# Kernel optimization log

Hardware: AMD Instinct MI355X
Metric: run time of the kernel (lower is better)

Reference implementation:

```python
import jax, jax.numpy as jnp
import numpy as np

B, S, E, H, DH, F, L, C = 32, 197, 768, 12, 64, 2048, 4, 1000
LN_EPS = 1e-5


def setup_inputs() -> dict:
    key = jax.random.key(0)
    ks = jax.random.split(key, 16)
    sc = 0.02
    return {
        "x": jax.random.normal(ks[0], (B, S, E), dtype=jnp.float32),
        "Wk": jax.random.normal(ks[1], (L, H, E, DH), dtype=jnp.float32) * sc,
        "Wq": jax.random.normal(ks[2], (L, H, E, DH), dtype=jnp.float32) * sc,
        "Wv": jax.random.normal(ks[3], (L, H, E, DH), dtype=jnp.float32) * sc,
        "Wconv": jax.random.normal(ks[4], (L, H * DH, E), dtype=jnp.float32) * sc,
        "ln1_w": jnp.ones((L, E), jnp.float32),
        "ln1_b": jnp.zeros((L, E), jnp.float32),
        "ln2_w": jnp.ones((L, E), jnp.float32),
        "ln2_b": jnp.zeros((L, E), jnp.float32),
        "W1": jax.random.normal(ks[5], (L, E, F), dtype=jnp.float32) * sc,
        "b1": jnp.zeros((L, F), jnp.float32),
        "W2": jax.random.normal(ks[6], (L, F, E), dtype=jnp.float32) * sc,
        "b2": jnp.zeros((L, E), jnp.float32),
        "Wc": jax.random.normal(ks[7], (E, C), dtype=jnp.float32) * sc,
        "bc": jnp.zeros((C,), jnp.float32),
    }


def _layernorm(x, w, b):
    mu = jnp.mean(x, axis=-1, keepdims=True)
    var = jnp.mean(jnp.square(x - mu), axis=-1, keepdims=True)
    return (x - mu) * jax.lax.rsqrt(var + LN_EPS) * w + b


def reference(x, Wk, Wq, Wv, Wconv, ln1_w, ln1_b, ln2_w, ln2_b, W1, b1, W2, b2, Wc, bc):
    # NOTE: original scales attention scores by sqrt(seq_len), not sqrt(d_k)
    seq_len = x.shape[1]
    inv_scale = 1.0 / jnp.sqrt(jnp.float32(seq_len))
    h = x
    for l in range(L):  # small fixed layer loop
        xn = _layernorm(h, ln1_w[l], ln1_b[l])
        q = jnp.einsum('bse,hed->bhsd', xn, Wq[l])
        k = jnp.einsum('bse,hed->bhsd', xn, Wk[l])
        v = jnp.einsum('bse,hed->bhsd', xn, Wv[l])
        scores = jnp.einsum('bhsd,bhtd->bhst', q, k) * inv_scale
        att = jax.nn.softmax(scores, axis=-1)
        o = jnp.einsum('bhst,bhtd->bhsd', att, v)
        # concat heads: b s (h d), head index outermost in last dim
        o = o.transpose(0, 2, 1, 3).reshape(o.shape[0], o.shape[2], H * DH)
        mha = o @ Wconv[l]
        res1 = mha + h
        xn2 = _layernorm(res1, ln2_w[l], ln2_b[l])
        ff = jax.nn.gelu(xn2 @ W1[l] + b1[l], approximate=False) @ W2[l] + b2[l]
        h = ff + res1
    logits = h[:, 0] @ Wc + bc
    return jax.nn.softmax(logits, axis=-1)
```

## Files before the change

### kernel.cpp

```cpp
#include <hip/hip_runtime.h>
#include <hip/hip_bf16.h>
#include <math.h>

#define BQ 32
#define SQ 197
#define EQ 768
#define HQ 12
#define DHQ 64
#define FQ 2048
#define LQ 4
#define CQ 1000
#define BSQ (BQ*SQ)
#define SP 208
#define S16 13
#define MP (BQ*SP)
#define QKV3 2304
#define KTP 7
#define LN_EPS 1e-5f

typedef __bf16 bf16x8 __attribute__((ext_vector_type(8)));
typedef float f32x4 __attribute__((ext_vector_type(4)));
typedef unsigned short u16x8 __attribute__((ext_vector_type(8)));

typedef const __attribute__((address_space(1))) unsigned int* gas_t;
typedef __attribute__((address_space(3))) unsigned int* las_t;

__device__ __forceinline__ __hip_bfloat16 tobf(float f) { return __float2bfloat16(f); }

__device__ __forceinline__ size_t pk(int rt, int KT, int kt, int lane) {
    return (((size_t)rt * KT + kt) * 64 + (size_t)lane) * 8;
}

#define QPK_SLAB (S16*2*512)
#define QPK_TOT  ((size_t)BQ*HQ*QPK_SLAB + 4096)
#define VPK_SLAB (4*KTP*512)
#define VPK_TOT  ((size_t)BQ*HQ*VPK_SLAB + 4096)
#define LWSLAB (4*(size_t)EQ*EQ + 2*(size_t)EQ*FQ)

template<int N>
__device__ __forceinline__ void waitvm() {
    asm volatile("s_waitcnt vmcnt(%0)" :: "n"(N) : "memory");
}
__device__ __forceinline__ void barx() {
    asm volatile("" ::: "memory");
    __builtin_amdgcn_s_barrier();
    asm volatile("" ::: "memory");
}
__device__ __forceinline__ void lds_fence() {
    asm volatile("s_waitcnt lgkmcnt(0)" ::: "memory");
    __builtin_amdgcn_sched_barrier(0);
}

__device__ __forceinline__ float gelu_f(float v) {
    float ax = fabsf(v) * 0.70710678118654752f;
    float t  = __builtin_amdgcn_rcpf(1.0f + 0.3275911f * ax);
    float p  = ((((1.061405429f * t - 1.453152027f) * t + 1.421413741f) * t
               - 0.284496736f) * t + 0.254829592f) * t;
    float e  = __expf(-ax * ax);
    float er = 1.0f - p * e;
    return v * (0.5f * (1.0f + copysignf(er, v)));
}

__global__ __launch_bounds__(256) void copy_pad(const float* __restrict__ x,
    float* __restrict__ bh)
{
    int r = blockIdx.x;
    int b = r / SP, s = r - b * SP;
    float* dst = bh + (size_t)r * EQ;
    int t = threadIdx.x;
    if (s < SQ) {
        const float* src = x + ((size_t)b * SQ + s) * EQ;
        dst[t]       = src[t];
        dst[t + 256] = src[t + 256];
        dst[t + 512] = src[t + 512];
    } else {
        dst[t] = 0.f; dst[t + 256] = 0.f; dst[t + 512] = 0.f;
    }
}

__device__ __forceinline__ void tconv_body(const float* __restrict__ ip,
    unsigned short* __restrict__ out, int C, int KT, int ntb_base, int r0, int c0)
{
    __shared__ float tile[64][65];
    int t = threadIdx.x;
    int tc = t & 63, tr = t >> 6;
    #pragma unroll
    for (int p = 0; p < 16; ++p) {
        int r = p * 4 + tr;
        tile[r][tc] = ip[(size_t)(r0 + r) * C + c0 + tc];
    }
    __syncthreads();
    int ntb = ntb_base + (c0 >> 4);
    int ktb = r0 >> 5;
    #pragma unroll
    for (int p = 0; p < 2; ++p) {
        int cc = p * 256 + t;
        int lane = cc & 63, grp = cc >> 6;
        int ktl = grp & 1, ntl = grp >> 1;
        int er = ktl * 32 + (lane >> 4) * 8;
        int dc = ntl * 16 + (lane & 15);
        u16x8 v;
        #pragma unroll
        for (int e = 0; e < 8; ++e) {
            __hip_bfloat16 h = tobf(tile[er + e][dc]);
            v[e] = *(unsigned short*)&h;
        }
        *(u16x8*)(out + pk(ntb + ntl, KT, ktb + ktl, lane)) = v;
    }
}

__global__ __launch_bounds__(256) void tconv_all(
    const float* __restrict__ Wq, const float* __restrict__ Wk,
    const float* __restrict__ Wv, const float* __restrict__ Wcv,
    const float* __restrict__ W1, const float* __restrict__ W2,
    unsigned short* __restrict__ wAll)
{
    int id = blockIdx.x;
    const int l = id / 1344; id -= l * 1344;
    unsigned short* wl = wAll + (size_t)l * LWSLAB;
    const float* src; unsigned short* dst;
    int C, KT, ntb, r0, c0;
    if (id < 432) {
        int x = id % 12, z = id / 12;
        int which = z / 12, zz = z - which * 12;
        const float* s0 = (which == 0) ? Wq : (which == 1) ? Wk : Wv;
        src = s0 + ((size_t)l * HQ + zz) * EQ * DHQ;
        dst = wl + (size_t)which * EQ * EQ;
        C = DHQ; KT = 24; ntb = zz * 4; r0 = x * 64; c0 = 0;
    } else if (id < 576) {
        int t = id - 432;
        src = Wcv + (size_t)l * EQ * EQ;
        dst = wl + 3 * (size_t)EQ * EQ;
        C = EQ; KT = 24; ntb = 0; r0 = (t % 12) * 64; c0 = (t / 12) * 64;
    } else if (id < 960) {
        int t = id - 576;
        src = W1 + (size_t)l * EQ * FQ;
        dst = wl + 4 * (size_t)EQ * EQ;
        C = FQ; KT = 24; ntb = 0; r0 = (t % 12) * 64; c0 = (t / 12) * 64;
    } else {
        int t = id - 960;
        src = W2 + (size_t)l * FQ * EQ;
        dst = wl + 4 * (size_t)EQ * EQ + (size_t)EQ * FQ;
        C = EQ; KT = 64; ntb = 0; r0 = (t % 32) * 64; c0 = (t / 32) * 64;
    }
    tconv_body(src, dst, C, KT, ntb, r0, c0);
}

__global__ __launch_bounds__(256) void ln_kernel(const float* __restrict__ in,
    const float* __restrict__ w, const float* __restrict__ b,
    unsigned short* __restrict__ out)
{
    const int wv = threadIdx.x >> 6, L = threadIdx.x & 63;
    const int row = blockIdx.x * 4 + wv;
    const float* x = in + (size_t)row * EQ;
    float4 a0 = *(const float4*)(x + 8 * L);
    float4 a1 = *(const float4*)(x + 8 * L + 4);
    float4 a2 = make_float4(0.f, 0.f, 0.f, 0.f), a3 = a2;
    const bool two = (L < 32);
    if (two) {
        a2 = *(const float4*)(x + 512 + 8 * L);
        a3 = *(const float4*)(x + 512 + 8 * L + 4);
    }
    float s = a0.x + a0.y + a0.z + a0.w + a1.x + a1.y + a1.z + a1.w
            + a2.x + a2.y + a2.z + a2.w + a3.x + a3.y + a3.z + a3.w;
    #pragma unroll
    for (int d = 1; d < 64; d <<= 1) s += __shfl_xor(s, d);
    const float mu = s * (1.0f / EQ);
    float q = (a0.x-mu)*(a0.x-mu) + (a0.y-mu)*(a0.y-mu) + (a0.z-mu)*(a0.z-mu) + (a0.w-mu)*(a0.w-mu)
            + (a1.x-mu)*(a1.x-mu) + (a1.y-mu)*(a1.y-mu) + (a1.z-mu)*(a1.z-mu) + (a1.w-mu)*(a1.w-mu);
    if (two)
        q += (a2.x-mu)*(a2.x-mu) + (a2.y-mu)*(a2.y-mu) + (a2.z-mu)*(a2.z-mu) + (a2.w-mu)*(a2.w-mu)
           + (a3.x-mu)*(a3.x-mu) + (a3.y-mu)*(a3.y-mu) + (a3.z-mu)*(a3.z-mu) + (a3.w-mu)*(a3.w-mu);
    #pragma unroll
    for (int d = 1; d < 64; d <<= 1) q += __shfl_xor(q, d);
    const float rs = rsqrtf(q * (1.0f / EQ) + LN_EPS);

    const int rt = row >> 4, rsl = row & 15;
    auto store_chunk = [&](int c, float4 v0, float4 v1) {
        int kt = c >> 2, c2 = c & 3;
        int lane2 = (c2 << 4) + rsl;
        int k0 = c << 3;
        float4 w0 = *(const float4*)(w + k0), w1 = *(const float4*)(w + k0 + 4);
        float4 g0 = *(const float4*)(b + k0), g1 = *(const float4*)(b + k0 + 4);
        float va[8] = {v0.x, v0.y, v0.z, v0.w, v1.x, v1.y, v1.z, v1.w};
        float wa[8] = {w0.x, w0.y, w0.z, w0.w, w1.x, w1.y, w1.z, w1.w};
        float ba[8] = {g0.x, g0.y, g0.z, g0.w, g1.x, g1.y, g1.z, g1.w};
        u16x8 o;
        #pragma unroll
        for (int e = 0; e < 8; ++e) {
            __hip_bfloat16 h = tobf((va[e] - mu) * rs * wa[e] + ba[e]);
            o[e] = *(unsigned short*)&h;
        }
        *(u16x8*)(out + pk(rt, 24, kt, lane2)) = o;
    };
    store_chunk(L, a0, a1);
    if (two) store_chunk(64 + L, a2, a3);
}

template<int KT, int RT>
__device__ __forceinline__ void kloop_staged(
    const unsigned short* __restrict__ Apk,
    const unsigned short* __restrict__ Bpk,
    int rtb, int ntb, int tid, unsigned short* sm, f32x4 (&acc)[RT][4])
{
    static_assert(KT >= 3, "need >=3 k-tiles");
    constexpr int AC  = RT * 2;
    constexpr int NCH = AC + 8;
    constexpr int CPW = NCH / 4;
    const int lane = tid & 63, w = tid >> 6;
    const int wr = w >> 1, wc = w & 1;
    const int cbase = w * CPW;

    const unsigned short* sp[CPW];
    #pragma unroll
    for (int q = 0; q < CPW; ++q) {
        int c = cbase + q;
        sp[q] = (c < AC) ? Apk + pk(rtb + c, KT, 0, lane)
                         : Bpk + pk(ntb + (c - AC), KT, 0, lane);
    }
    unsigned short* bufs0 = sm;
    unsigned short* bufs1 = sm + NCH * 512;
    unsigned short* bufs2 = sm + 2 * NCH * 512;

    auto stagef = [&](unsigned short* dst) {
        #pragma unroll
        for (int q = 0; q < CPW; ++q) {
            __builtin_amdgcn_global_load_lds(
                (gas_t)sp[q], (las_t)(dst + (cbase + q) * 512), 16, 0, 0);
            sp[q] += 512;
        }
    };
    auto frags = [&](const unsigned short* cur, bf16x8 (&af)[RT], bf16x8 (&bb)[4]) {
        #pragma unroll
        for (int i = 0; i < RT; ++i)
            af[i] = *(const bf16x8*)(cur + (wr * RT + i) * 512 + lane * 8);
        #pragma unroll
        for (int j = 0; j < 4; ++j)
            bb[j] = *(const bf16x8*)(cur + (AC + wc * 4 + j) * 512 + lane * 8);
    };
    auto mf = [&](bf16x8 (&af)[RT], bf16x8 (&bb)[4]) {
        #pragma unroll
        for (int i = 0; i < RT; ++i)
            #pragma unroll
            for (int j = 0; j < 4; ++j)
                acc[i][j] = __builtin_amdgcn_mfma_f32_16x16x32_bf16(af[i], bb[j], acc[i][j], 0, 0, 0);
    };

    stagef(bufs0);
    stagef(bufs1);
    unsigned short *cur = bufs0, *nxt = bufs1, *nx2 = bufs2;

    #pragma unroll 1
    for (int kt = 0; kt < KT - 2; ++kt) {
        waitvm<CPW>();
        barx();
        bf16x8 af[RT], bb[4];
        frags(cur, af, bb);
        stagef(nx2);
        mf(af, bb);
        unsigned short* t_ = cur; cur = nxt; nxt = nx2; nx2 = t_;
    }
    {
        waitvm<CPW>();
        barx();
        bf16x8 af[RT], bb[4];
        frags(cur, af, bb);
        mf(af, bb);
        cur = nxt;
    }
    {
        waitvm<0>();
        barx();
        bf16x8 af[RT], bb[4];
        frags(cur, af, bb);
        mf(af, bb);
    }
}

enum { EPI_NONE = 0, EPI_RES = 1, EPI_BIAS_GELU = 2, EPI_BIAS_RES = 3, EPI_QKV = 4 };

template<int EPI, int KT, int RT>
__global__ __launch_bounds__(256, 3) void mgemm_pk(
    const unsigned short* __restrict__ Apk, const unsigned short* __restrict__ Bpk,
    void* __restrict__ Cm, const float* __restrict__ bias,
    const float* __restrict__ res, int N, int nNT)
{
    constexpr int NCH = RT * 2 + 8;
    __shared__ __align__(16) unsigned short smem[(3 * NCH * 1024) / 2];

    const int nRowT = (RT == 4) ? 52 : 104;
    const int g = blockIdx.x & 7;
    const int sIdx = blockIdx.x >> 3;
    const int b0 = (nRowT * g) >> 3, b1 = (nRowT * (g + 1)) >> 3;
    const int colT = sIdx % nNT, rloc = sIdx / nNT;
    if (b0 + rloc >= b1) return;
    const int row0 = (b0 + rloc) * (RT * 32), col0 = colT << 7;

    const int tid = threadIdx.x;
    const int lane = tid & 63;
    const int w = tid >> 6;
    const int wr = w >> 1, wc = w & 1;
    const int l15 = lane & 15, quad = lane >> 4;

    f32x4 acc[RT][4] = {};
    kloop_staged<KT, RT>(Apk, Bpk, row0 >> 4, col0 >> 4, tid, smem, acc);

    if constexpr (EPI == EPI_BIAS_GELU) {
        __syncthreads();
        auto Cs = (unsigned short (*)[136])smem;
        #pragma unroll
        for (int j = 0; j < 4; ++j) {
            float bv = bias[col0 + wc * 64 + j * 16 + l15];
            #pragma unroll
            for (int i = 0; i < RT; ++i)
                #pragma unroll
                for (int rg = 0; rg < 4; ++rg) {
                    float v = gelu_f(acc[i][j][rg] + bv);
                    __hip_bfloat16 h = tobf(v);
                    Cs[wr * 64 + i * 16 + quad * 4 + rg][wc * 64 + j * 16 + l15] =
                        *(unsigned short*)&h;
                }
        }
        __syncthreads();
        const int KT2 = N >> 5;
        #pragma unroll
        for (int p = 0; p < 8; ++p) {
            int cc = p * 256 + tid;
            int ln2 = cc & 63, grp = cc >> 6;
            int ktl = grp & 3, rtl = grp >> 2;
            int rowl = rtl * 16 + (ln2 & 15);
            u16x8 v;
            #pragma unroll
            for (int e = 0; e < 8; ++e)
                v[e] = Cs[rowl][ktl * 32 + (ln2 >> 4) * 8 + e];
            *(u16x8*)((unsigned short*)Cm + pk((row0 >> 4) + rtl, KT2, (col0 >> 5) + ktl, ln2)) = v;
        }
    } else if constexpr (EPI == EPI_QKV) {
        unsigned short* qpk = (unsigned short*)Cm;
        unsigned short* kpk = (unsigned short*)(void*)bias;
        unsigned short* vpk = (unsigned short*)(void*)res;
        __syncthreads();
        auto Cs = (unsigned short (*)[136])smem;
        #pragma unroll
        for (int j = 0; j < 4; ++j)
            #pragma unroll
            for (int i = 0; i < 4; ++i)
                #pragma unroll
                for (int rg = 0; rg < 4; ++rg) {
                    __hip_bfloat16 h = tobf(acc[i][j][rg]);
                    Cs[wr * 64 + i * 16 + quad * 4 + rg][wc * 64 + j * 16 + l15] =
                        *(unsigned short*)&h;
                }
        __syncthreads();

        const int treg = col0 >> 7;
        if (treg < 12) {
            unsigned short* dst = (treg < 6) ? qpk : kpk;
            const int h0 = ((col0 % 768) >> 6);
            #pragma unroll
            for (int p = 0; p < 8; ++p) {
                int cc = p * 256 + tid;
                int ln2 = cc & 63, grp = cc >> 6;
                int hl = grp & 1, kt = (grp >> 1) & 1, rtl = grp >> 2;
                int row16 = (row0 >> 4) + rtl;
                int bb = row16 / S16;
                int s16 = row16 - bb * S16;
                int h = h0 + hl;
                u16x8 v;
                #pragma unroll
                for (int e = 0; e < 8; ++e)
                    v[e] = Cs[rtl * 16 + (ln2 & 15)][hl * 64 + kt * 32 + (ln2 >> 4) * 8 + e];
                *(u16x8*)(dst + ((((size_t)(bb * HQ + h) * S16 + s16) * 2 + kt) << 9) + ln2 * 8) = v;
            }
        } else {
            const int h0 = (col0 - 1536) >> 6;
            #pragma unroll
            for (int p = 0; p < 8; ++p) {
                int cc = p * 256 + tid;
                int dloc = cc & 127;
                int g8 = cc >> 7;
                int gr = row0 + g8 * 8;
                int bb = gr / SP;
                int tl = gr - bb * SP;
                int tt = tl >> 5;
                int tsub = (tl >> 3) & 3;
                int h = h0 + (dloc >> 6);
                int dt = (dloc >> 4) & 3;
                int lane2 = tsub * 16 + (dloc & 15);
                u16x8 v;
                #pragma unroll
                for (int e = 0; e < 8; ++e)
                    v[e] = Cs[g8 * 8 + e][dloc];
                *(u16x8*)(vpk + (size_t)(bb * HQ + h) * VPK_SLAB + pk(dt, KTP, tt, lane2)) = v;
            }
        }
    } else {
        #pragma unroll
        for (int j = 0; j < 4; ++j) {
            int c = col0 + wc * 64 + j * 16 + l15;
            float bv = (EPI == EPI_BIAS_RES) ? bias[c] : 0.f;
            #pragma unroll
            for (int i = 0; i < RT; ++i)
                #pragma unroll
                for (int rg = 0; rg < 4; ++rg) {
                    int r = row0 + wr * (RT * 16) + i * 16 + quad * 4 + rg;
                    float v = acc[i][j][rg];
                    size_t idx = (size_t)r * N + c;
                    if (EPI == EPI_BIAS_RES) {
                        ((float*)Cm)[idx] = v + bv + res[idx];
                    } else if (EPI == EPI_RES) {
                        ((float*)Cm)[idx] = v + res[idx];
                    } else {
                        ((__hip_bfloat16*)Cm)[idx] = tobf(v);
                    }
                }
        }
    }
}

__global__ __launch_bounds__(128, 4) void attn_fused(
    const unsigned short* __restrict__ qpk, const unsigned short* __restrict__ kpk,
    const unsigned short* __restrict__ vpk, unsigned short* __restrict__ opk)
{
    __shared__ unsigned short Ps[2][16][240];
    __shared__ unsigned short Cs[2][16][72];
    const int bh = blockIdx.x;
    const int b = bh / HQ, h = bh - b * HQ;
    const int tid = threadIdx.x;
    const int w = tid >> 6, lane = tid & 63;
    const int l15 = lane & 15, quad = lane >> 4;
    const int rt = blockIdx.y * 2 + w;
    if (rt >= S16) return;

    const unsigned short* qs = qpk + (size_t)bh * QPK_SLAB;
    const unsigned short* ks = kpk + (size_t)bh * QPK_SLAB;
    const unsigned short* vs = vpk + (size_t)bh * VPK_SLAB;

    bf16x8 af0 = *(const bf16x8*)(qs + ((rt * 2 + 0) << 9) + lane * 8);
    bf16x8 af1 = *(const bf16x8*)(qs + ((rt * 2 + 1) << 9) + lane * 8);

    f32x4 acc[13] = {};
    bf16x8 kc0 = *(const bf16x8*)(ks + (0 << 9) + lane * 8);
    bf16x8 kc1 = *(const bf16x8*)(ks + (1 << 9) + lane * 8);
    #pragma unroll
    for (int j = 0; j < 13; ++j) {
        bf16x8 kn0, kn1;
        if (j + 1 < 13) {
            kn0 = *(const bf16x8*)(ks + (((j + 1) * 2 + 0) << 9) + lane * 8);
            kn1 = *(const bf16x8*)(ks + (((j + 1) * 2 + 1) << 9) + lane * 8);
        }
        __builtin_amdgcn_s_setprio(1);
        acc[j] = __builtin_amdgcn_mfma_f32_16x16x32_bf16(af0, kc0, acc[j], 0, 0, 0);
        acc[j] = __builtin_amdgcn_mfma_f32_16x16x32_bf16(af1, kc1, acc[j], 0, 0, 0);
        __builtin_amdgcn_s_setprio(0);
        kc0 = kn0; kc1 = kn1;
    }

    bf16x8 vb[4];
    #pragma unroll
    for (int d = 0; d < 4; ++d)
        vb[d] = *(const bf16x8*)(vs + pk(d, KTP, 0, lane));

    const float scale = 0.07124704998790965f;
    const int xr = (quad & 2) << 3;
    const unsigned short zbf = 0;
    float inv[4];
    #pragma unroll
    for (int rg = 0; rg < 4; ++rg) {
        float y[13];
        float m = -1e30f;
        #pragma unroll
        for (int j = 0; j < 13; ++j) {
            float v = acc[j][rg] * scale;
            if (j == 12) v = (l15 < 5) ? v : -1e30f;
            y[j] = v;
            m = fmaxf(m, v);
        }
        #pragma unroll
        for (int d = 1; d < 16; d <<= 1) m = fmaxf(m, __shfl_xor(m, d));
        float s = 0.f;
        #pragma unroll
        for (int j = 0; j < 13; ++j) {
            float e = __expf(y[j] - m);
            s += e;
            __hip_bfloat16 hv = tobf(e);
            Ps[w][quad * 4 + rg][(j * 16 + l15) ^ xr] = *(unsigned short*)&hv;
        }
        Ps[w][quad * 4 + rg][(208 + l15) ^ xr] = zbf;
        #pragma unroll
        for (int d = 1; d < 16; d <<= 1) s += __shfl_xor(s, d);
        inv[rg] = 1.0f / s;
    }
    lds_fence();

    f32x4 av[4] = {};
    #pragma unroll
    for (int kk = 0; kk < KTP; ++kk) {
        bf16x8 vn[4];
        if (kk + 1 < KTP) {
            #pragma unroll
            for (int d = 0; d < 4; ++d)
                vn[d] = *(const bf16x8*)(vs + pk(d, KTP, kk + 1, lane));
        }
        int col = (kk * 32 + quad * 8) ^ ((l15 & 8) << 1);
        bf16x8 pf = *(const bf16x8*)&Ps[w][l15][col];
        __builtin_amdgcn_s_setprio(1);
        #pragma unroll
        for (int d = 0; d < 4; ++d)
            av[d] = __builtin_amdgcn_mfma_f32_16x16x32_bf16(pf, vb[d], av[d], 0, 0, 0);
        __builtin_amdgcn_s_setprio(0);
        #pragma unroll
        for (int d = 0; d < 4; ++d) vb[d] = vn[d];
    }

    #pragma unroll
    for (int d = 0; d < 4; ++d)
        #pragma unroll
        for (int rg = 0; rg < 4; ++rg) {
            __hip_bfloat16 hv = tobf(av[d][rg] * inv[rg]);
            Cs[w][quad * 4 + rg][d * 16 + l15] = *(unsigned short*)&hv;
        }
    lds_fence();

    const int rtg = b * S16 + rt;
    #pragma unroll
    for (int ktl = 0; ktl < 2; ++ktl) {
        u16x8 v;
        #pragma unroll
        for (int e = 0; e < 8; ++e)
            v[e] = Cs[w][l15][ktl * 32 + quad * 8 + e];
        *(u16x8*)(opk + pk(rtg, 24, h * 2 + ktl, lane)) = v;
    }
}

__global__ __launch_bounds__(256) void logits_kernel(
    const float* __restrict__ hbuf, const float* __restrict__ Wc,
    const float* __restrict__ bc, float* __restrict__ logits)
{
    __shared__ __align__(16) float hs[768];
    __shared__ float red[256];
    int b = blockIdx.y;
    int tid = threadIdx.x;
    const float* hr = hbuf + (size_t)b * SP * EQ;
    for (int p = tid; p < 192; p += 256)
        *(float4*)&hs[p << 2] = *(const float4*)(hr + (p << 2));
    __syncthreads();
    int cl = tid & 31, ks = tid >> 5;
    int c = blockIdx.x * 32 + cl;
    int cs = (c < CQ) ? c : 0;
    float s = 0.f;
    int e0 = ks * 96;
    #pragma unroll 8
    for (int e = 0; e < 96; ++e)
        s = fmaf(hs[e0 + e], Wc[(size_t)(e0 + e) * CQ + cs], s);
    red[tid] = s;
    __syncthreads();
    for (int off = 128; off >= 32; off >>= 1) {
        if (tid < off) red[tid] += red[tid + off];
        __syncthreads();
    }
    if (tid < 32 && c < CQ)
        logits[(size_t)b * CQ + c] = red[tid] + bc[c];
}

__global__ __launch_bounds__(256) void smax_kernel(
    const float* __restrict__ logits, float* __restrict__ out)
{
    __shared__ float red[256];
    int b = blockIdx.x;
    int t = threadIdx.x;
    const float* lp = logits + (size_t)b * CQ;
    float lg[4];
    #pragma unroll
    for (int j = 0; j < 4; ++j) {
        int c = t + j * 256;
        lg[j] = (c < CQ) ? lp[c] : -1e30f;
    }
    float m = fmaxf(fmaxf(lg[0], lg[1]), fmaxf(lg[2], lg[3]));
    red[t] = m;
    __syncthreads();
    for (int off = 128; off; off >>= 1) {
        if (t < off) red[t] = fmaxf(red[t], red[t + off]);
        __syncthreads();
    }
    m = red[0];
    __syncthreads();
    float ex[4], s = 0.f;
    #pragma unroll
    for (int j = 0; j < 4; ++j) {
        ex[j] = (t + j * 256 < CQ) ? __expf(lg[j] - m) : 0.f;
        s += ex[j];
    }
    red[t] = s;
    __syncthreads();
    for (int off = 128; off; off >>= 1) {
        if (t < off) red[t] += red[t + off];
        __syncthreads();
    }
    float inv = 1.0f / red[0];
    #pragma unroll
    for (int j = 0; j < 4; ++j)
        if (t + j * 256 < CQ) out[(size_t)b * CQ + t + j * 256] = ex[j] * inv;
}

extern "C" void kernel_launch(void* const* d_in, const int* in_sizes, int n_in,
                              void* d_out, int out_size, void* d_ws, size_t ws_size,
                              hipStream_t stream)
{
    const float* x     = (const float*)d_in[0];
    const float* Wk    = (const float*)d_in[1];
    const float* Wq    = (const float*)d_in[2];
    const float* Wv    = (const float*)d_in[3];
    const float* Wconv = (const float*)d_in[4];
    const float* ln1w  = (const float*)d_in[5];
    const float* ln1b  = (const float*)d_in[6];
    const float* ln2w  = (const float*)d_in[7];
    const float* ln2b  = (const float*)d_in[8];
    const float* W1    = (const float*)d_in[9];
    const float* b1    = (const float*)d_in[10];
    const float* W2    = (const float*)d_in[11];
    const float* b2    = (const float*)d_in[12];
    const float* Wc    = (const float*)d_in[13];
    const float* bc    = (const float*)d_in[14];
    float* out = (float*)d_out;

    const size_t MPE = (size_t)MP * EQ;

    float* w = (float*)d_ws;
    float* bh    = w; w += MPE;
    float* res1  = w; w += MPE;
    float* logit = w; w += (size_t)BQ * CQ;
    unsigned short* qpk  = (unsigned short*)w;
    unsigned short* kpk  = qpk + QPK_TOT;
    unsigned short* vpk  = kpk + QPK_TOT;
    unsigned short* actb = vpk + VPK_TOT;
    unsigned short* ffh  = actb + MPE;
    unsigned short* wAll = ffh + (size_t)MP * FQ;

    copy_pad<<<MP, 256, 0, stream>>>(x, bh);
    tconv_all<<<4 * 1344, 256, 0, stream>>>(Wq, Wk, Wv, Wconv, W1, W2, wAll);

    for (int l = 0; l < LQ; ++l) {
        unsigned short* wl   = wAll + (size_t)l * LWSLAB;
        unsigned short* WcvT = wl + 3 * (size_t)EQ * EQ;
        unsigned short* W1T  = wl + 4 * (size_t)EQ * EQ;
        unsigned short* W2T  = W1T + (size_t)EQ * FQ;

        ln_kernel<<<MP / 4, 256, 0, stream>>>(bh, ln1w + l * EQ, ln1b + l * EQ, actb);

        mgemm_pk<EPI_QKV, 24, 4><<<8 * 7 * 18, 256, 0, stream>>>(
            actb, wl, qpk, (const float*)kpk, (const float*)vpk, QKV3, 18);

        attn_fused<<<dim3(BQ * HQ, 7), 128, 0, stream>>>(qpk, kpk, vpk, actb);

        mgemm_pk<EPI_RES, 24, 2><<<8 * 13 * 6, 256, 0, stream>>>(
            actb, WcvT, res1, nullptr, bh, EQ, 6);

        ln_kernel<<<MP / 4, 256, 0, stream>>>(res1, ln2w + l * EQ, ln2b + l * EQ, actb);

        mgemm_pk<EPI_BIAS_GELU, 24, 4><<<8 * 7 * 16, 256, 0, stream>>>(
            actb, W1T, ffh, b1 + l * FQ, nullptr, FQ, 16);
        mgemm_pk<EPI_BIAS_RES, 64, 2><<<8 * 13 * 6, 256, 0, stream>>>(
            ffh, W2T, bh, b2 + l * EQ, res1, EQ, 6);
    }
    logits_kernel<<<dim3(32, BQ), 256, 0, stream>>>(bh, Wc, bc, logit);
    smax_kernel<<<BQ, 256, 0, stream>>>(logit, out);
}
```

Measured before the change: 710.5 us.

## Add 512x128-tile GEMM kernel with triple-buffered LDS staging for QKV and FFN1

Adds a new GEMM kernel using 512-thread blocks that compute a 512x128 output tile. It stages A and B chunks into LDS with direct global-to-LDS loads and a three-deep buffer ring, and the epilogue is written out in four 128-row bands through shared memory. The QKV projection and the first FFN GEMM now use this kernel instead of the 128-row-tile kernel, with the aim of reusing each weight tile across more rows and cutting global reads of B. In exchange there are far fewer blocks (234 and 208), large LDS use and heavy register pressure from 32 accumulators per wave, which can hurt occupancy and load balance.

```diff
diff --git a/kernel.cpp b/kernel.cpp
--- a/kernel.cpp
+++ b/kernel.cpp
@@ -305,116 +305,198 @@
     f32x4 acc[RT][4] = {};
     kloop_staged<KT, RT>(Apk, Bpk, row0 >> 4, col0 >> 4, tid, smem, acc);
 
-    if constexpr (EPI == EPI_BIAS_GELU) {
+    #pragma unroll
+    for (int j = 0; j < 4; ++j) {
+        int c = col0 + wc * 64 + j * 16 + l15;
+        float bv = (EPI == EPI_BIAS_RES) ? bias[c] : 0.f;
+        #pragma unroll
+        for (int i = 0; i < RT; ++i)
+            #pragma unroll
+            for (int rg = 0; rg < 4; ++rg) {
+                int r = row0 + wr * (RT * 16) + i * 16 + quad * 4 + rg;
+                float v = acc[i][j][rg];
+                size_t idx = (size_t)r * N + c;
+                if (EPI == EPI_BIAS_RES) {
+                    ((float*)Cm)[idx] = v + bv + res[idx];
+                } else if (EPI == EPI_RES) {
+                    ((float*)Cm)[idx] = v + res[idx];
+                } else {
+                    ((__hip_bfloat16*)Cm)[idx] = tobf(v);
+                }
+            }
+    }
+}
+
+template<int EPI, int KT>
+__global__ __launch_bounds__(512, 2) void mgemm_big(
+    const unsigned short* __restrict__ Apk, const unsigned short* __restrict__ Bpk,
+    void* __restrict__ Cm, const float* __restrict__ bias,
+    const float* __restrict__ res, int N, int nNT)
+{
+    constexpr int NCH = 40;
+    __shared__ __align__(16) unsigned short smem[3 * NCH * 512];
+
+    const int sIdx = blockIdx.x;
+    const int colT = sIdx % nNT, mt = sIdx / nNT;
+    const int row0 = mt << 9, col0 = colT << 7;
+
+    const int tid = threadIdx.x;
+    const int lane = tid & 63;
+    const int w = tid >> 6;
+    const int wr = w >> 1, wc = w & 1;
+    const int l15 = lane & 15, quad = lane >> 4;
+    const int rtb = row0 >> 4, ntb = col0 >> 4;
+
+    const unsigned short* sp[5];
+    #pragma unroll
+    for (int q = 0; q < 5; ++q) {
+        int c = w * 5 + q;
+        sp[q] = (c < 32) ? Apk + pk(rtb + c, KT, 0, lane)
+                         : Bpk + pk(ntb + (c - 32), KT, 0, lane);
+    }
+    unsigned short* bufs0 = smem;
+    unsigned short* bufs1 = smem + NCH * 512;
+    unsigned short* bufs2 = smem + 2 * NCH * 512;
+
+    auto stagef = [&](unsigned short* dst) {
+        #pragma unroll
+        for (int q = 0; q < 5; ++q) {
+            __builtin_amdgcn_global_load_lds(
+                (gas_t)sp[q], (las_t)(dst + (w * 5 + q) * 512), 16, 0, 0);
+            sp[q] += 512;
+        }
+    };
+    f32x4 acc[8][4] = {};
+    auto ldfrags = [&](const unsigned short* cur, bf16x8 (&af)[8], bf16x8 (&bb)[4]) {
+        #pragma unroll
+        for (int i = 0; i < 8; ++i)
+            af[i] = *(const bf16x8*)(cur + (wr * 8 + i) * 512 + lane * 8);
+        #pragma unroll
+        for (int j = 0; j < 4; ++j)
+            bb[j] = *(const bf16x8*)(cur + (32 + wc * 4 + j) * 512 + lane * 8);
+    };
+    auto domfma = [&](bf16x8 (&af)[8], bf16x8 (&bb)[4]) {
+        __builtin_amdgcn_s_setprio(1);
+        #pragma unroll
+        for (int i = 0; i < 8; ++i)
+            #pragma unroll
+            for (int j = 0; j < 4; ++j)
+                acc[i][j] = __builtin_amdgcn_mfma_f32_16x16x32_bf16(af[i], bb[j], acc[i][j], 0, 0, 0);
+        __builtin_amdgcn_s_setprio(0);
+    };
+
+    stagef(bufs0);
+    stagef(bufs1);
+    unsigned short *cur = bufs0, *nxt = bufs1, *nx2 = bufs2;
+    #pragma unroll 1
+    for (int kt = 0; kt < KT - 2; ++kt) {
+        waitvm<5>();
+        barx();
+        bf16x8 af[8], bb[4];
+        ldfrags(cur, af, bb);
+        stagef(nx2);
+        domfma(af, bb);
+        unsigned short* t_ = cur; cur = nxt; nxt = nx2; nx2 = t_;
+    }
+    {
+        waitvm<5>();
+        barx();
+        bf16x8 af[8], bb[4];
+        ldfrags(cur, af, bb);
+        domfma(af, bb);
+        cur = nxt;
+    }
+    {
+        waitvm<0>();
+        barx();
+        bf16x8 af[8], bb[4];
+        ldfrags(cur, af, bb);
+        domfma(af, bb);
+    }
+
+    __syncthreads();
+    auto Cs = (unsigned short (*)[136])smem;
+    #pragma unroll 1
+    for (int band = 0; band < 4; ++band) {
+        if (wr == band) {
+            #pragma unroll
+            for (int j = 0; j < 4; ++j) {
+                float bv = (EPI == EPI_BIAS_GELU) ? bias[col0 + wc * 64 + j * 16 + l15] : 0.f;
+                #pragma unroll
+                for (int i = 0; i < 8; ++i)
+                    #pragma unroll
+                    for (int rg = 0; rg < 4; ++rg) {
+                        float v = acc[i][j][rg];
+                        if (EPI == EPI_BIAS_GELU) v = gelu_f(v + bv);
+                        __hip_bfloat16 h = tobf(v);
+                        Cs[i * 16 + quad * 4 + rg][wc * 64 + j * 16 + l15] =
+                            *(unsigned short*)&h;
+                    }
+            }
+        }
         __syncthreads();
-        auto Cs = (unsigned short (*)[136])smem;
-        #pragma unroll
-        for (int j = 0; j < 4; ++j) {
-            float bv = bias[col0 + wc * 64 + j * 16 + l15];
+        const int row0b = row0 + (band << 7);
+        if constexpr (EPI == EPI_BIAS_GELU) {
+            const int KT2 = N >> 5;
             #pragma unroll
-            for (int i = 0; i < RT; ++i)
-                #pragma unroll
-                for (int rg = 0; rg < 4; ++rg) {
-                    float v = gelu_f(acc[i][j][rg] + bv);
-                    __hip_bfloat16 h = tobf(v);
-                    Cs[wr * 64 + i * 16 + quad * 4 + rg][wc * 64 + j * 16 + l15] =
-                        *(unsigned short*)&h;
-                }
-        }
-        __syncthreads();
-        const int KT2 = N >> 5;
-        #pragma unroll
-        for (int p = 0; p < 8; ++p) {
-            int cc = p * 256 + tid;
-            int ln2 = cc & 63, grp = cc >> 6;
-            int ktl = grp & 3, rtl = grp >> 2;
-            int rowl = rtl * 16 + (ln2 & 15);
-            u16x8 v;
-            #pragma unroll
-            for (int e = 0; e < 8; ++e)
-                v[e] = Cs[rowl][ktl * 32 + (ln2 >> 4) * 8 + e];
-            *(u16x8*)((unsigned short*)Cm + pk((row0 >> 4) + rtl, KT2, (col0 >> 5) + ktl, ln2)) = v;
-        }
-    } else if constexpr (EPI == EPI_QKV) {
-        unsigned short* qpk = (unsigned short*)Cm;
-        unsigned short* kpk = (unsigned short*)(void*)bias;
-        unsigned short* vpk = (unsigned short*)(void*)res;
-        __syncthreads();
-        auto Cs = (unsigned short (*)[136])smem;
-        #pragma unroll
-        for (int j = 0; j < 4; ++j)
-            #pragma unroll
-            for (int i = 0; i < 4; ++i)
-                #pragma unroll
-                for (int rg = 0; rg < 4; ++rg) {
-                    __hip_bfloat16 h = tobf(acc[i][j][rg]);
-                    Cs[wr * 64 + i * 16 + quad * 4 + rg][wc * 64 + j * 16 + l15] =
-                        *(unsigned short*)&h;
-                }
-        __syncthreads();
-
-        const int treg = col0 >> 7;
-        if (treg < 12) {
-            unsigned short* dst = (treg < 6) ? qpk : kpk;
-            const int h0 = ((col0 % 768) >> 6);
-            #pragma unroll
-            for (int p = 0; p < 8; ++p) {
-                int cc = p * 256 + tid;
+            for (int p = 0; p < 4; ++p) {
+                int cc = p * 512 + tid;
                 int ln2 = cc & 63, grp = cc >> 6;
-                int hl = grp & 1, kt = (grp >> 1) & 1, rtl = grp >> 2;
-                int row16 = (row0 >> 4) + rtl;
-                int bb = row16 / S16;
-                int s16 = row16 - bb * S16;
-                int h = h0 + hl;
+                int ktl = grp & 3, rtl = grp >> 2;
+                int rowl = rtl * 16 + (ln2 & 15);
                 u16x8 v;
                 #pragma unroll
                 for (int e = 0; e < 8; ++e)
-                    v[e] = Cs[rtl * 16 + (ln2 & 15)][hl * 64 + kt * 32 + (ln2 >> 4) * 8 + e];
-                *(u16x8*)(dst + ((((size_t)(bb * HQ + h) * S16 + s16) * 2 + kt) << 9) + ln2 * 8) = v;
+                    v[e] = Cs[rowl][ktl * 32 + (ln2 >> 4) * 8 + e];
+                *(u16x8*)((unsigned short*)Cm + pk((row0b >> 4) + rtl, KT2, (col0 >> 5) + ktl, ln2)) = v;
             }
         } else {
-            const int h0 = (col0 - 1536) >> 6;
-            #pragma unroll
-            for (int p = 0; p < 8; ++p) {
-                int cc = p * 256 + tid;
-                int dloc = cc & 127;
-                int g8 = cc >> 7;
-                int gr = row0 + g8 * 8;
-                int bb = gr / SP;
-                int tl = gr - bb * SP;
-                int tt = tl >> 5;
-                int tsub = (tl >> 3) & 3;
-                int h = h0 + (dloc >> 6);
-                int dt = (dloc >> 4) & 3;
-                int lane2 = tsub * 16 + (dloc & 15);
-                u16x8 v;
+            unsigned short* qpkO = (unsigned short*)Cm;
+            unsigned short* kpkO = (unsigned short*)(void*)bias;
+            unsigned short* vpkO = (unsigned short*)(void*)res;
+            const int treg = col0 >> 7;
+            if (treg < 12) {
+                unsigned short* dst = (treg < 6) ? qpkO : kpkO;
+                const int h0 = ((col0 % 768) >> 6);
                 #pragma unroll
-                for (int e = 0; e < 8; ++e)
-                    v[e] = Cs[g8 * 8 + e][dloc];
-                *(u16x8*)(vpk + (size_t)(bb * HQ + h) * VPK_SLAB + pk(dt, KTP, tt, lane2)) = v;
+                for (int p = 0; p < 4; ++p) {
+                    int cc = p * 512 + tid;
+                    int ln2 = cc & 63, grp = cc >> 6;
+                    int hl = grp & 1, kt2 = (grp >> 1) & 1, rtl = grp >> 2;
+                    int row16 = (row0b >> 4) + rtl;
+                    int bb2 = row16 / S16;
+                    int s16 = row16 - bb2 * S16;
+                    int hh = h0 + hl;
+                    u16x8 v;
+                    #pragma unroll
+                    for (int e = 0; e < 8; ++e)
+                        v[e] = Cs[rtl * 16 + (ln2 & 15)][hl * 64 + kt2 * 32 + (ln2 >> 4) * 8 + e];
+                    *(u16x8*)(dst + ((((size_t)(bb2 * HQ + hh) * S16 + s16) * 2 + kt2) << 9) + ln2 * 8) = v;
+                }
+            } else {
+                const int h0 = (col0 - 1536) >> 6;
+                #pragma unroll
+                for (int p = 0; p < 4; ++p) {
+                    int cc = p * 512 + tid;
+                    int dloc = cc & 127;
+                    int g8 = cc >> 7;
+                    int gr = row0b + g8 * 8;
+                    int bb2 = gr / SP;
+                    int tl = gr - bb2 * SP;
+                    int tt = tl >> 5;
+                    int tsub = (tl >> 3) & 3;
+                    int hh = h0 + (dloc >> 6);
+                    int dt = (dloc >> 4) & 3;
+                    int lane2 = tsub * 16 + (dloc & 15);
+                    u16x8 v;
+                    #pragma unroll
+                    for (int e = 0; e < 8; ++e)
+                        v[e] = Cs[g8 * 8 + e][dloc];
+                    *(u16x8*)(vpkO + (size_t)(bb2 * HQ + hh) * VPK_SLAB + pk(dt, KTP, tt, lane2)) = v;
+                }
             }
         }
-    } else {
-        #pragma unroll
-        for (int j = 0; j < 4; ++j) {
-            int c = col0 + wc * 64 + j * 16 + l15;
-            float bv = (EPI == EPI_BIAS_RES) ? bias[c] : 0.f;
-            #pragma unroll
-            for (int i = 0; i < RT; ++i)
-                #pragma unroll
-                for (int rg = 0; rg < 4; ++rg) {
-                    int r = row0 + wr * (RT * 16) + i * 16 + quad * 4 + rg;
-                    float v = acc[i][j][rg];
-                    size_t idx = (size_t)r * N + c;
-                    if (EPI == EPI_BIAS_RES) {
-                        ((float*)Cm)[idx] = v + bv + res[idx];
-                    } else if (EPI == EPI_RES) {
-                        ((float*)Cm)[idx] = v + res[idx];
-                    } else {
-                        ((__hip_bfloat16*)Cm)[idx] = tobf(v);
-                    }
-                }
-        }
+        __syncthreads();
     }
 }
 
@@ -648,7 +730,7 @@
 
         ln_kernel<<<MP / 4, 256, 0, stream>>>(bh, ln1w + l * EQ, ln1b + l * EQ, actb);
 
-        mgemm_pk<EPI_QKV, 24, 4><<<8 * 7 * 18, 256, 0, stream>>>(
+        mgemm_big<EPI_QKV, 24><<<13 * 18, 512, 0, stream>>>(
             actb, wl, qpk, (const float*)kpk, (const float*)vpk, QKV3, 18);
 
         attn_fused<<<dim3(BQ * HQ, 7), 128, 0, stream>>>(qpk, kpk, vpk, actb);
@@ -658,7 +740,7 @@
 
         ln_kernel<<<MP / 4, 256, 0, stream>>>(res1, ln2w + l * EQ, ln2b + l * EQ, actb);
 
-        mgemm_pk<EPI_BIAS_GELU, 24, 4><<<8 * 7 * 16, 256, 0, stream>>>(
+        mgemm_big<EPI_BIAS_GELU, 24><<<13 * 16, 512, 0, stream>>>(
             actb, W1T, ffh, b1 + l * FQ, nullptr, FQ, 16);
         mgemm_pk<EPI_BIAS_RES, 64, 2><<<8 * 13 * 6, 256, 0, stream>>>(
             ffh, W2T, bh, b2 + l * EQ, res1, EQ, 6);
```

After: 785.4 us. +10.5%, slower.
